# Performance work log

Hardware: AMD Instinct MI355X
Metric: run time of the kernel (lower is better)

Reference implementation:

```python
import jax, jax.numpy as jnp
import numpy as np

B, D, C, N = 8, 49, 512, 12
BN_EPS = 1e-5
SCALE = (C // 2) ** -0.5


def bn_train(x, axes):
    # training-mode batchnorm, gamma=1 beta=0 (per bn_init / default init)
    m = jnp.mean(x, axis=axes, keepdims=True)
    v = jnp.var(x, axis=axes, keepdims=True)
    return (x - m) * jax.lax.rsqrt(v + BN_EPS)


def l2norm(x):
    n = jnp.linalg.norm(x, axis=-1, keepdims=True)
    return x / jnp.maximum(n, 1e-12)


def cross_attn(y, xkv, wq, bq, wk, bk, wv, bv):
    q = y @ wq + bq
    k = xkv @ wk + bk
    v = xkv @ wv + bv
    a = jax.nn.softmax(jnp.einsum('...ik,...jk->...ij', q, k) * SCALE, axis=-1)
    return a @ v


def _gnn_layer(xv, ed, wa, wb, we, wu, wv):
    # incidence-matrix einsums reduce to repeat (end-gather) / tile (start-gather)
    res = xv
    agg = jnp.repeat(xv @ wa, N, axis=1) + jnp.tile(xv @ wb, (1, N, 1)) + ed @ we
    ed = ed + jax.nn.relu(bn_train(agg, (0, 2)))
    e = jax.nn.sigmoid(ed).reshape(-1, N, N, C)
    e = jax.nn.softmax(e, axis=2).reshape(-1, N * N, C)
    uj = jnp.tile(xv @ wv, (1, N, 1))
    msg = (e * uj).reshape(-1, N, N, C).sum(axis=2) / N  # scatter via end.T
    xv = jax.nn.relu(res + bn_train(xv @ wu + msg, (0, 2)))
    return xv, ed


def setup_inputs() -> dict:
    ks = iter(jax.random.split(jax.random.key(0), 64))

    def nrm(shape, scale=0.02):
        return jax.random.normal(next(ks), shape, dtype=jnp.float32) * scale

    g = float(np.sqrt(2.0 / C))
    inp = {'x': jax.random.normal(next(ks), (B, D, C), dtype=jnp.float32)}
    inp['Wc'] = nrm((N, C, C))
    inp['bc'] = nrm((N, C), 0.01)
    for p in ('fam', 'arm'):
        inp[p + '_wq'] = nrm((C, C // 2))
        inp[p + '_bq'] = nrm((C // 2,), 0.01)
        inp[p + '_wk'] = nrm((C, C // 2))
        inp[p + '_bk'] = nrm((C // 2,), 0.01)
        inp[p + '_wv'] = nrm((C, C))
        inp[p + '_bv'] = nrm((C,), 0.01)
    inp['ep_w'] = nrm((C, C))
    inp['ep_b'] = nrm((C,), 0.01)
    for nm in ('g_wa1', 'g_wb1', 'g_we1', 'g_wu1', 'g_wv1',
               'g_wa2', 'g_wb2', 'g_we2', 'g_wu2', 'g_wv2'):
        inp[nm] = nrm((C, C), g)
    inp['sc'] = nrm((N, C), float(np.sqrt(6.0 / (N + C))))
    inp['efc_w'] = nrm((C, 4), float(np.sqrt(6.0 / (C + 4))))
    inp['efc_b'] = nrm((4,), 0.01)
    return inp


def reference(x, Wc, bc,
              fam_wq, fam_bq, fam_wk, fam_bk, fam_wv, fam_bv,
              arm_wq, arm_bq, arm_wk, arm_bk, arm_wv, arm_bv,
              ep_w, ep_b,
              g_wa1, g_wb1, g_we1, g_wu1, g_wv1,
              g_wa2, g_wb2, g_we2, g_wu2, g_wv2,
              sc, efc_w, efc_b):
    b = x.shape[0]
    # per-class LinearBlocks (fc -> BN -> ReLU), vectorized over classes
    h = jnp.einsum('bdc,nco->bndo', x, Wc) + bc[None, :, None, :]
    f_u = jax.nn.relu(bn_train(h, (0, 2)))          # (b, N, D, C)
    f_v = f_u.mean(axis=2)                           # (b, N, C)
    # GEM edge extractor
    gf = jnp.broadcast_to(x[:, None], (b, N, D, C))
    feat = cross_attn(f_u, gf, fam_wq, fam_bq, fam_wk, fam_bk, fam_wv, fam_bv)
    feat_end = jnp.repeat(feat, N, axis=1)           # (b, N*N, D, C): edge (i,j) -> node i
    feat_start = jnp.tile(feat, (1, N, 1, 1))        # edge (i,j) -> node j
    feat = cross_attn(feat_start, feat_end, arm_wq, arm_bq, arm_wk, arm_bk, arm_wv, arm_bv)
    f_e = bn_train(feat @ ep_w + ep_b, (0, 2, 3)).mean(axis=2)  # (b, N*N, C)
    # cosine-similarity adjacency mask (detached), digraph-normalized
    si = l2norm(jax.lax.stop_gradient(f_v))
    adj = jnp.einsum('bik,bjk->bij', si, si)
    dis = jnp.sum(adj, axis=-1) ** -0.5
    mask = (adj * dis[:, :, None] * dis[:, None, :]).reshape(b, N * N, 1)
    f_e = f_e * mask
    # two GNN message-passing layers
    f_v, f_e = _gnn_layer(f_v, f_e, g_wa1, g_wb1, g_we1, g_wu1, g_wv1)
    f_v, f_e = _gnn_layer(f_v, f_e, g_wa2, g_wb2, g_we2, g_wu2, g_wv2)
    # cosine classifier + edge fc
    scn = l2norm(jax.nn.relu(sc))
    cl = jnp.sum(l2norm(f_v) * scn[None], axis=-1)   # (b, N)
    cl_edge = f_e @ efc_w + efc_b                    # (b, N*N, 4)
    return cl, cl_edge
```

## Files before the change

kernel.cpp:

```cpp
#include <hip/hip_runtime.h>
#include <math.h>

namespace {

constexpr int B = 8, D = 49, C = 512, N = 12, H = 256, E = 144;
constexpr int M_BD  = B * D;
constexpr int M_BND = B * N * D;
constexpr float BN_EPS = 1e-5f;
constexpr float ATT_SCALE = 0.0625f;

typedef __attribute__((ext_vector_type(4))) float  floatx4;
typedef __attribute__((ext_vector_type(8))) short  shortx8;

__device__ inline unsigned short f2bf(float f) {
  unsigned u = __float_as_uint(f);
  return (unsigned short)((u + 0x7fffu + ((u >> 16) & 1u)) >> 16);
}
__device__ inline float bf2f(unsigned short u) {
  return __uint_as_float(((unsigned)u) << 16);
}

__device__ inline void gload16(const unsigned short* g, unsigned short* l) {
  __builtin_amdgcn_global_load_lds(
      (const __attribute__((address_space(1))) void*)g,
      (__attribute__((address_space(3))) void*)l, 16, 0, 0);
}

struct TCJobs {
  const float* src[28];
  unsigned short* dst[28];
  int nn[28];
};

__global__ __launch_bounds__(256)
void tcast_k(TCJobs jobs)
{
  const int z = blockIdx.z;
  const float* src = jobs.src[z];
  unsigned short* dst = jobs.dst[z];
  const int Nn = jobs.nn[z];
  const int tx = blockIdx.x, ty = blockIdx.y;
  if (tx * 32 >= Nn) return;
  __shared__ float t[32][33];
  const int tid = threadIdx.x;
  const int lr = tid >> 5, lc = tid & 31;
#pragma unroll
  for (int p = 0; p < 4; ++p) {
    int k = ty * 32 + p * 8 + lr;
    t[p * 8 + lr][lc] = src[(long long)k * Nn + tx * 32 + lc];
  }
  __syncthreads();
#pragma unroll
  for (int p = 0; p < 4; ++p) {
    int n = tx * 32 + p * 8 + lr;
    dst[(long long)n * 512 + ty * 32 + lc] = f2bf(t[lc][p * 8 + lr]);
  }
}

__global__ __launch_bounds__(256)
void castrow_k(const float* __restrict__ x, unsigned short* __restrict__ xb,
               const float* __restrict__ awv, unsigned short* __restrict__ armwvb,
               const float* __restrict__ bk, const float* __restrict__ bv,
               const float* __restrict__ bq2, const float* __restrict__ bk2,
               const float* __restrict__ arm_bv, const float* __restrict__ epw,
               const float* __restrict__ epb,
               float* __restrict__ kvbias, float* __restrict__ qkvbias)
{
  int idx = blockIdx.x * 256 + threadIdx.x;
  const int n1 = M_BD * C / 8;
  const int n2 = n1 + C * C / 8;
  if (idx < n1) {
    int i8 = idx * 8;
    float4 a = *reinterpret_cast<const float4*>(x + i8);
    float4 b = *reinterpret_cast<const float4*>(x + i8 + 4);
    shortx8 o;
    o[0]=(short)f2bf(a.x); o[1]=(short)f2bf(a.y); o[2]=(short)f2bf(a.z); o[3]=(short)f2bf(a.w);
    o[4]=(short)f2bf(b.x); o[5]=(short)f2bf(b.y); o[6]=(short)f2bf(b.z); o[7]=(short)f2bf(b.w);
    *reinterpret_cast<shortx8*>(xb + i8) = o;
  } else if (idx < n2) {
    int i8 = (idx - n1) * 8;
    float4 a = *reinterpret_cast<const float4*>(awv + i8);
    float4 b = *reinterpret_cast<const float4*>(awv + i8 + 4);
    shortx8 o;
    o[0]=(short)f2bf(a.x); o[1]=(short)f2bf(a.y); o[2]=(short)f2bf(a.z); o[3]=(short)f2bf(a.w);
    o[4]=(short)f2bf(b.x); o[5]=(short)f2bf(b.y); o[6]=(short)f2bf(b.z); o[7]=(short)f2bf(b.w);
    *reinterpret_cast<shortx8*>(armwvb + i8) = o;
  } else if (idx >= 58112 && idx < 58624) {
    int c = idx - 58112;
    float s = epb[c];
    for (int k = 0; k < C; ++k) s = fmaf(arm_bv[k], epw[k * C + c], s);
    qkvbias[512 + c] = s;
  }
  if (idx < 256) { kvbias[idx] = bk[idx]; qkvbias[idx] = bq2[idx]; qkvbias[256 + idx] = bk2[idx]; }
  if (idx < 512) kvbias[256 + idx] = bv[idx];
}

__device__ __forceinline__
void gemm64_body(const void* __restrict__ Ain, const unsigned short* __restrict__ Bt,
                 const float* __restrict__ bp, float* __restrict__ co,
                 unsigned short* __restrict__ cb,
                 int M, int Nn, int K, int lda, int ldb, int ldc, int abf,
                 int bx, int by)
{
  const float* Af = abf ? nullptr : (const float*)Ain;
  const unsigned short* Ab = abf ? (const unsigned short*)Ain : nullptr;

  __shared__ short As[64 * 72];
  __shared__ short Bs[64 * 72];

  const int tid = threadIdx.x;
  const int row0 = bx * 64, col0 = by * 64;
  const int wid = tid >> 6, lane = tid & 63;
  const int wr = wid >> 1, wc = wid & 1;
  const int lr = lane & 15, lg = lane >> 4;

  floatx4 acc00 = {0.f,0.f,0.f,0.f}, acc01 = {0.f,0.f,0.f,0.f};
  floatx4 acc10 = {0.f,0.f,0.f,0.f}, acc11 = {0.f,0.f,0.f,0.f};

  const int r = tid >> 2, seg = tid & 3;
  const int gr = row0 + r, gn = col0 + r;
  short* aw = &As[r * 72 + seg * 16];
  short* bw = &Bs[r * 72 + seg * 16];
  const shortx8 zz = {0,0,0,0,0,0,0,0};

  for (int k0 = 0; k0 < K; k0 += 64) {
    shortx8 w0, w1;
    if (gr < M) {
      if (abf) {
        const shortx8* ap = reinterpret_cast<const shortx8*>(Ab + (long long)gr * lda + seg * 16 + k0);
        w0 = ap[0]; w1 = ap[1];
      } else {
        const float4* ap = reinterpret_cast<const float4*>(Af + (long long)gr * lda + seg * 16 + k0);
        float4 fa0 = ap[0], fa1 = ap[1], fa2 = ap[2], fa3 = ap[3];
        w0[0]=(short)f2bf(fa0.x); w0[1]=(short)f2bf(fa0.y); w0[2]=(short)f2bf(fa0.z); w0[3]=(short)f2bf(fa0.w);
        w0[4]=(short)f2bf(fa1.x); w0[5]=(short)f2bf(fa1.y); w0[6]=(short)f2bf(fa1.z); w0[7]=(short)f2bf(fa1.w);
        w1[0]=(short)f2bf(fa2.x); w1[1]=(short)f2bf(fa2.y); w1[2]=(short)f2bf(fa2.z); w1[3]=(short)f2bf(fa2.w);
        w1[4]=(short)f2bf(fa3.x); w1[5]=(short)f2bf(fa3.y); w1[6]=(short)f2bf(fa3.z); w1[7]=(short)f2bf(fa3.w);
      }
    } else { w0 = zz; w1 = zz; }
    const shortx8* bp8 = reinterpret_cast<const shortx8*>(Bt + (long long)gn * ldb + seg * 16 + k0);
    shortx8 b0v = bp8[0];
    shortx8 b1v = bp8[1];

    __syncthreads();
    *reinterpret_cast<shortx8*>(aw)     = w0;
    *reinterpret_cast<shortx8*>(aw + 8) = w1;
    *reinterpret_cast<shortx8*>(bw)     = b0v;
// ... 30 lines not shown
                if (okB) co[(long long)ra * ldc + colB] = v01; }
      if (cb) { if (okA) cb[(long long)ra * ldc + colA] = f2bf(v00);
                if (okB) cb[(long long)ra * ldc + colB] = f2bf(v01); }
    }
    if (rb < M) {
      if (co) { if (okA) co[(long long)rb * ldc + colA] = v10;
                if (okB) co[(long long)rb * ldc + colB] = v11; }
      if (cb) { if (okA) cb[(long long)rb * ldc + colA] = f2bf(v10);
                if (okB) cb[(long long)rb * ldc + colB] = f2bf(v11); }
    }
  }
}

__global__ __launch_bounds__(256)
void gemm_mfma(const void* __restrict__ Ain, const unsigned short* __restrict__ Bt,
               const float* __restrict__ bias, float* __restrict__ Co,
               unsigned short* __restrict__ Cb,
               int M, int Nn, int K, int lda, int ldb, int ldc, int abf,
               long long sA, long long sB, long long sBias, long long sC)
{
  const int z = blockIdx.z;
  const void* A = abf ? (const void*)((const unsigned short*)Ain + z * sA)
                      : (const void*)((const float*)Ain + z * sA);
  gemm64_body(A, Bt + z * sB, bias ? bias + z * sBias : nullptr,
              Co ? Co + z * sC : nullptr, Cb ? Cb + z * sC : nullptr,
              M, Nn, K, lda, ldb, ldc, abf, blockIdx.x, blockIdx.y);
}

struct GJob {
  const void* A; const unsigned short* B; const float* bias;
  float* Co; unsigned short* Cb;
  int M, Nn, K, lda, ldb, ldc, abf, tx;
};
struct GJobs { GJob j[3]; int ends[3]; int n; };

__global__ __launch_bounds__(256)
void gemm_jobs(GJobs js)
{
  const int bid = blockIdx.x;
#pragma unroll
  for (int q = 0; q < 3; ++q) {
    if (q < js.n && bid < js.ends[q]) {
      int start = q ? js.ends[q - 1] : 0;
      int local = bid - start;
      const GJob& J = js.j[q];
      gemm64_body(J.A, J.B, J.bias, J.Co, J.Cb,
                  J.M, J.Nn, J.K, J.lda, J.ldb, J.ldc, J.abf,
                  local % J.tx, local / J.tx);
      return;
    }
  }
}

__global__ __launch_bounds__(256)
void gemm128g(const unsigned short* __restrict__ Ab, const unsigned short* __restrict__ Bt,
              const float* __restrict__ bias, float* __restrict__ Co,
              unsigned short* __restrict__ Cb,
              int M, int Nn, int K, int lda, int ldb, int ldc,
              long long sA, long long sB, long long sBias, long long sC)
{
  const int z = blockIdx.z;
  Ab += z * sA; Bt += z * sB;
  float* co = Co ? Co + z * sC : nullptr;
  unsigned short* cb = Cb ? Cb + z * sC : nullptr;
  const float* bp = bias ? bias + z * sBias : nullptr;

  __shared__ unsigned short As[128 * 64];
  __shared__ unsigned short Bs[128 * 64];

  const int tid = threadIdx.x;
  const int row0 = blockIdx.x * 128, col0 = blockIdx.y * 128;
  const int wid = tid >> 6, lane = tid & 63;
  const int wr = wid >> 1, wc = wid & 1;
  const int lr = lane & 15, lg = lane >> 4;

  floatx4 acc[4][4];
#pragma unroll
  for (int mf = 0; mf < 4; ++mf)
#pragma unroll
    for (int nf = 0; nf < 4; ++nf) acc[mf][nf] = floatx4{0.f,0.f,0.f,0.f};

  const int rsub = tid >> 3;
  const int csub = (tid & 7) * 8;

  for (int k0 = 0; k0 < K; k0 += 64) {
    __syncthreads();
#pragma unroll
    for (int it = 0; it < 4; ++it) {
      int r = it * 32 + rsub;
      gload16(Ab + (long long)(row0 + r) * lda + k0 + csub, As + it * 2048 + tid * 8);
      gload16(Bt + (long long)(col0 + r) * ldb + k0 + csub, Bs + it * 2048 + tid * 8);
    }
    __syncthreads();

#pragma unroll
    for (int kt = 0; kt < 2; ++kt) {
      shortx8 af[4], bf[4];
#pragma unroll
      for (int mf = 0; mf < 4; ++mf)
        af[mf] = *reinterpret_cast<const shortx8*>(&As[(wr*64 + mf*16 + lr) * 64 + kt*32 + lg*8]);
#pragma unroll
      for (int nf = 0; nf < 4; ++nf)
        bf[nf] = *reinterpret_cast<const shortx8*>(&Bs[(wc*64 + nf*16 + lr) * 64 + kt*32 + lg*8]);
#pragma unroll
      for (int mf = 0; mf < 4; ++mf)
#pragma unroll
        for (int nf = 0; nf < 4; ++nf)
          acc[mf][nf] = __builtin_amdgcn_mfma_f32_16x16x32_bf16(af[mf], bf[nf], acc[mf][nf], 0, 0, 0);
    }
  }

#pragma unroll
  for (int nf = 0; nf < 4; ++nf) {
    const int col = col0 + wc * 64 + nf * 16 + lr;
    if (col >= Nn) continue;
    const float bv = bp ? bp[col] : 0.f;
#pragma unroll
    for (int mf = 0; mf < 4; ++mf) {
      const int rbase = row0 + wr * 64 + mf * 16 + lg * 4;
#pragma unroll
      for (int jj = 0; jj < 4; ++jj) {
        int row = rbase + jj;
        if (row >= M) continue;
        float v = acc[mf][nf][jj] + bv;
        if (co) co[(long long)row * ldc + col] = v;
        if (cb) cb[(long long)row * ldc + col] = f2bf(v);
      }
    }
  }
}

__global__ __launch_bounds__(256)
void bn_stats_part(const float* __restrict__ h, float* __restrict__ ps,
                   float* __restrict__ pq)
{
  int idx = blockIdx.x * 256 + threadIdx.x;
  int n = idx >> 9, c = idx & 511;
  int slice = blockIdx.y;
  const float* p = h + (long long)n * M_BD * C + (long long)slice * 49 * C + c;
  float s = 0.f, q = 0.f;
  for (int rr = 0; rr < 49; ++rr) { float v = p[(long long)rr * C]; s += v; q += v * v; }
  ps[slice * (N * C) + idx] = s;
  pq[slice * (N * C) + idx] = q;
}

__global__ __launch_bounds__(256)
void fu_fv(const float* __restrict__ h, const float* __restrict__ ps,
           const float* __restrict__ pq, unsigned short* __restrict__ fub,
           float* __restrict__ fv)
{
  const int bid = blockIdx.x;
  const int b = bid / N, n = bid % N;
  const int c = blockIdx.y * 256 + threadIdx.x;
  const int idx = n * C + c;
  float s = 0.f, q = 0.f;
#pragma unroll
  for (int sl = 0; sl < 8; ++sl) { s += ps[sl * (N * C) + idx]; q += pq[sl * (N * C) + idx]; }
  float m = s / (float)M_BD;
  float rv = rsqrtf(q / (float)M_BD - m * m + BN_EPS);
  float acc = 0.f;
  for (int d = 0; d < D; ++d) {
    float v = h[((long long)n * M_BD + b * D + d) * C + c];
    v = fmaxf((v - m) * rv, 0.f);
    fub[((long long)bid * D + d) * C + c] = f2bf(v);
    acc += v;
  }
  fv[(long long)bid * C + c] = acc * (1.0f / (float)D);
}

__global__ __launch_bounds__(256)
void softvxt_k(const float* __restrict__ Sf, unsigned short* __restrict__ Ppb,
               const unsigned short* __restrict__ kvx, unsigned short* __restrict__ vxtb)
{
  const int tid = threadIdx.x;
  if (blockIdx.x < 19) {
    int row = blockIdx.x * 256 + tid;
    if (row >= M_BND) return;
    const float* p = Sf + (long long)row * 49;
    float v[49];
    float m = -1e30f;
#pragma unroll
    for (int j = 0; j < 49; ++j) { v[j] = p[j] * ATT_SCALE; m = fmaxf(m, v[j]); }
    float s = 0.f;
#pragma unroll
    for (int j = 0; j < 49; ++j) { v[j] = __expf(v[j] - m); s += v[j]; }
    float inv = 1.f / s;
    unsigned short* o = Ppb + (long long)row * 64;
#pragma unroll
    for (int j = 0; j < 49; ++j) o[j] = f2bf(v[j] * inv);
#pragma unroll
    for (int j = 49; j < 64; ++j) o[j] = 0;
    return;
  }
  const int i = blockIdx.x - 19;
  const int b = i >> 3, cc = i & 7;
  __shared__ unsigned short t[49][65];
  for (int idx = tid; idx < 49 * 64; idx += 256) {
    int rr = idx >> 6, k = idx & 63;
    t[rr][k] = kvx[(long long)(b * 49 + rr) * 768 + 256 + cc * 64 + k];
  }
  __syncthreads();
  for (int idx = tid; idx < 64 * 64; idx += 256) {
    int n = idx >> 6, kk = idx & 63;
    vxtb[((long long)b * 512 + cc * 64 + n) * 64 + kk] = (kk < 49) ? t[kk][n] : (unsigned short)0;
  }
}

__global__ __launch_bounds__(256)
void edge_finish(const float* __restrict__ Sc, const float* __restrict__ G,
                 const unsigned short* __restrict__ qkvfe,
                 float* __restrict__ S1, float* __restrict__ eS)
{
  const int bid = blockIdx.x;
  const int b = bid / E, e = bid % E;
  const int i = e / N, j = e % N;
  const float* Scb = Sc + (long long)b * 588 * 588 + (long long)(j * 49) * 588 + i * 49;
  const float* Gp  = G + (long long)(b * N + i) * 2401;
  const unsigned short* Vp = qkvfe + (long long)(b * N + i) * D * 1024 + 512;

  __shared__ float aT[49][53];
  __shared__ float g[49][53];
  __shared__ unsigned short abT[64][72];
  __shared__ float ws[52];
  __shared__ float r0[4], r1[4];
  const int tid = threadIdx.x;
  const int wid = tid >> 6, lane = tid & 63;
  const int lr = lane & 15, lg = lane >> 4;

  for (int idx = tid; idx < 49 * 49; idx += 256) {
    int di = idx / 49, dj = idx - di * 49;
    aT[dj][di] = Scb[di * 588 + dj] * ATT_SCALE;
    g[di][dj] = Gp[idx];
  }
  __syncthreads();
  if (tid < D) {
    float m = -1e30f;
    for (int jj = 0; jj < D; ++jj) m = fmaxf(m, aT[jj][tid]);
    float s = 0.f;
    for (int jj = 0; jj < D; ++jj) { float ev = __expf(aT[jj][tid] - m); aT[jj][tid] = ev; s += ev; }
    float inv = 1.f / s;
    for (int jj = 0; jj < D; ++jj) aT[jj][tid] *= inv;
  }
  __syncthreads();
  for (int idx = tid; idx < 64 * 64; idx += 256) {
    int dj = idx >> 6, di = idx & 63;
    float v = (dj < D && di < D) ? aT[dj][di] : 0.f;
    abT[dj][di] = f2bf(v);
  }
  if (tid < D) {
    float s = 0.f;
    for (int di = 0; di < D; ++di) s += aT[tid][di];
    ws[tid] = s;
  }
  __syncthreads();

  floatx4 acc[4];
#pragma unroll
  for (int tk = 0; tk < 4; ++tk) acc[tk] = floatx4{0.f,0.f,0.f,0.f};
  shortx8 af0 = *reinterpret_cast<const shortx8*>(&abT[wid * 16 + lr][lg * 8]);
  shortx8 af1 = *reinterpret_cast<const shortx8*>(&abT[wid * 16 + lr][32 + lg * 8]);
#pragma unroll
  for (int tk = 0; tk < 4; ++tk) {
    shortx8 bf0v = *reinterpret_cast<const shortx8*>(&abT[tk * 16 + lr][lg * 8]);
    shortx8 bf1v = *reinterpret_cast<const shortx8*>(&abT[tk * 16 + lr][32 + lg * 8]);
    acc[tk] = __builtin_amdgcn_mfma_f32_16x16x32_bf16(af0, bf0v, acc[tk], 0, 0, 0);
    acc[tk] = __builtin_amdgcn_mfma_f32_16x16x32_bf16(af1, bf1v, acc[tk], 0, 0, 0);
  }
  float st2 = 0.f;
#pragma unroll
  for (int tk = 0; tk < 4; ++tk) {
    int kcol = tk * 16 + lr;
#pragma unroll
    for (int rg = 0; rg < 4; ++rg) {
      int jrow = wid * 16 + lg * 4 + rg;
      if (jrow < D && kcol < D) st2 = fmaf(acc[tk][rg], g[jrow][kcol], st2);
    }
  }

  float st = 0.f;
#pragma unroll
  for (int cc = 0; cc < C; cc += 256) {
    int cg = cc + tid;
    float s1 = 0.f;
    for (int dk = 0; dk < D; ++dk) s1 = fmaf(ws[dk], bf2f(Vp[dk * 1024 + cg]), s1);
    S1[(long long)bid * C + cg] = s1;
    st += s1;
  }
  for (int off = 32; off; off >>= 1) { st += __shfl_down(st, off); st2 += __shfl_down(st2, off); }
  if (lane == 0) { r0[wid] = st; r1[wid] = st2; }
  __syncthreads();
  if (tid == 0) {
    eS[bid * 2 + 0] = r0[0] + r0[1] + r0[2] + r0[3];
    eS[bid * 2 + 1] = r1[0] + r1[1] + r1[2] + r1[3];
  }
}

__global__ __launch_bounds__(256)
void mask_me_k(const float* __restrict__ fv, const float* __restrict__ eS,
               float* __restrict__ mask, float* __restrict__ me, float* __restrict__ rve)
{
  if (blockIdx.x == B) {
    int e = threadIdx.x;
    if (e < E) {
      float s = 0.f, q = 0.f;
      for (int b = 0; b < B; ++b) { s += eS[(b * E + e) * 2]; q += eS[(b * E + e) * 2 + 1]; }
      const float inv = 1.f / (float)(B * D * C);
      float m = s * inv;
      me[e] = m;
      rve[e] = rsqrtf(q * inv - m * m + BN_EPS);
    }
    return;
  }
  const int b = blockIdx.x;
  __shared__ float fl[N][C];
  __shared__ float adj[N][N];
  __shared__ float nrm[N];
  __shared__ float dis[N];
  const int tid = threadIdx.x;
  for (int idx = tid; idx < N * C; idx += 256)
    fl[idx / C][idx % C] = fv[(long long)b * N * C + idx];
  __syncthreads();
  if (tid < N * N) {
    int i = tid / N, j = tid % N;
    float s = 0.f;
    for (int k = 0; k < C; ++k) s += fl[i][k] * fl[j][k];
    adj[i][j] = s;
  }
  __syncthreads();
  if (tid < N) nrm[tid] = fmaxf(sqrtf(adj[tid][tid]), 1e-12f);
  __syncthreads();
  if (tid < N * N) {
    int i = tid / N, j = tid % N;
    adj[i][j] = adj[i][j] / (nrm[i] * nrm[j]);
  }
  __syncthreads();
  if (tid < N) {
    float s = 0.f;
    for (int j = 0; j < N; ++j) s += adj[tid][j];
    dis[tid] = rsqrtf(s);
  }
  __syncthreads();
  if (tid < N * N) {
    int i = tid / N, j = tid % N;
    mask[b * E + tid] = adj[i][j] * dis[i] * dis[j];
  }
}

__global__ void fe_k(const float* __restrict__ S1, const float* __restrict__ me,
                     const float* __restrict__ rve, const float* __restrict__ mask,
                     float* __restrict__ fe)
{
  long long idx = (long long)blockIdx.x * 256 + threadIdx.x;
  if (idx >= (long long)B * E * C) return;
  long long be = idx / C;
  int e = (int)(be % E);
  fe[idx] = (S1[idx] * (1.0f / (float)D) - me[e]) * rve[e] * mask[be];
}

__global__ __launch_bounds__(256)
void agg_stats(const float* __restrict__ ABUV, const float* __restrict__ EW,
               float* __restrict__ mu_e, float* __restrict__ rs_e)
{
  const int e = blockIdx.x;
  const int i = e / N, j = e % N;
  const int tid = threadIdx.x;
  float s = 0.f, q = 0.f;
  for (int idx = tid; idx < B * C; idx += 256) {
    int b = idx >> 9, c = idx & 511;
    float v = ABUV[(long long)(b * N + i) * 2048 + c]
            + ABUV[(long long)(b * N + j) * 2048 + 512 + c]
            + EW[((long long)b * E + e) * C + c];
    s += v; q += v * v;
  }
  for (int off = 32; off; off >>= 1) { s += __shfl_down(s, off); q += __shfl_down(q, off); }
  __shared__ float r0[4], r1[4];
  int wid = tid >> 6, lane = tid & 63;
  if (lane == 0) { r0[wid] = s; r1[wid] = q; }
  __syncthreads();
  if (tid == 0) {
    float ss = r0[0] + r0[1] + r0[2] + r0[3];
    float qq = r1[0] + r1[1] + r1[2] + r1[3];
    float m = ss / (float)(B * C);
    mu_e[e] = m;
    rs_e[e] = rsqrtf(qq / (float)(B * C) - m * m + BN_EPS);
  }
}

__global__ __launch_bounds__(256)
void edmsg_k(float* __restrict__ fe, const float* __restrict__ ABUV,
             const float* __restrict__ EW, const float* __restrict__ mu_e,
             const float* __restrict__ rs_e, float* __restrict__ pre)
{
  const int bid = blockIdx.x;
  const int b = bid / N, i = bid % N;
  const int tid = threadIdx.x;
  for (int c = tid; c < C; c += 256) {
    float ai = ABUV[(long long)(b * N + i) * 2048 + c];
    float sv[N];
    float m = -1e30f;
#pragma unroll
    for (int jn = 0; jn < N; ++jn) {
      int e = i * N + jn;
      float v = ai + ABUV[(long long)(b * N + jn) * 2048 + 512 + c]
              + EW[((long long)b * E + e) * C + c];
      v = (v - mu_e[e]) * rs_e[e];
      float ed = fe[((long long)b * E + e) * C + c] + fmaxf(v, 0.f);
      fe[((long long)b * E + e) * C + c] = ed;
      float sg = 1.f / (1.f + __expf(-ed));
      sv[jn] = sg; m = fmaxf(m, sg);
    }
    float sum = 0.f;
#pragma unroll
    for (int jn = 0; jn < N; ++jn) { float ev = __expf(sv[jn] - m); sv[jn] = ev; sum += ev; }
    float acc = 0.f;
#pragma unroll
    for (int jn = 0; jn < N; ++jn)
      acc = fmaf(sv[jn], ABUV[(long long)(b * N + jn) * 2048 + 1536 + c], acc);
    acc /= (sum * (float)N);
    pre[(long long)bid * C + c] = ABUV[(long long)bid * 2048 + 1024 + c] + acc;
  }
}

__global__ __launch_bounds__(256)
void node_part(const float* __restrict__ pre, float* __restrict__ nps,
               float* __restrict__ npq)
{
  const int i = blockIdx.x, b = blockIdx.y;
  const int tid = threadIdx.x;
  float v0 = pre[(long long)(b * N + i) * C + tid];
  float v1 = pre[(long long)(b * N + i) * C + 256 + tid];
  float s = v0 + v1, q = v0 * v0 + v1 * v1;
  for (int off = 32; off; off >>= 1) { s += __shfl_down(s, off); q += __shfl_down(q, off); }
  __shared__ float r0[4], r1[4];
  int wid = tid >> 6, lane = tid & 63;
  if (lane == 0) { r0[wid] = s; r1[wid] = q; }
  __syncthreads();
  if (tid == 0) {
    nps[i * B + b] = r0[0] + r0[1] + r0[2] + r0[3];
    npq[i * B + b] = r1[0] + r1[1] + r1[2] + r1[3];
  }
}

__global__ void xv_update(float* __restrict__ xv, const float* __restrict__ pre,
                          const float* __restrict__ nps, const float* __restrict__ npq)
{
  long long idx = (long long)blockIdx.x * 256 + threadIdx.x;
  if (idx >= (long long)B * N * C) return;
  int i = (int)((idx / C) % N);
  float s = 0.f, q = 0.f;
#pragma unroll
  for (int bb = 0; bb < B; ++bb) { s += nps[i * B + bb]; q += npq[i * B + bb]; }
  float mu = s * (1.f / (float)(B * C));
  float rs = rsqrtf(q * (1.f / (float)(B * C)) - mu * mu + BN_EPS);
  float v = xv[idx] + (pre[idx] - mu) * rs;
  xv[idx] = fmaxf(v, 0.f);
}

__global__ __launch_bounds__(256)
void out_k(const float* __restrict__ xv, const float* __restrict__ sc,
           const float* __restrict__ ed, const float* __restrict__ w,
           const float* __restrict__ bias, float* __restrict__ out)
{
  const int bid = blockIdx.x;
  const int tid = threadIdx.x;
  int wid = tid >> 6, lane = tid & 63;
  if (bid < B * N) {
    const int b = bid / N, i = bid % N;
    float sxx = 0.f, sss = 0.f, sxs = 0.f;
    for (int c = tid; c < C; c += 256) {
      float xvv = xv[(long long)(b * N + i) * C + c];
      float scv = fmaxf(sc[i * C + c], 0.f);
      sxx += xvv * xvv; sss += scv * scv; sxs += xvv * scv;
    }
    for (int off = 32; off; off >>= 1) {
      sxx += __shfl_down(sxx, off);
      sss += __shfl_down(sss, off);
      sxs += __shfl_down(sxs, off);
    }
    __shared__ float r0[4], r1[4], r2[4];
    if (lane == 0) { r0[wid] = sxx; r1[wid] = sss; r2[wid] = sxs; }
    __syncthreads();
    if (tid == 0) {
      float a = r0[0] + r0[1] + r0[2] + r0[3];
      float s = r1[0] + r1[1] + r1[2] + r1[3];
      float p = r2[0] + r2[1] + r2[2] + r2[3];
      float nx = fmaxf(sqrtf(a), 1e-12f);
      float ns = fmaxf(sqrtf(s), 1e-12f);
      out[b * N + i] = p / (nx * ns);
// ... 17 lines not shown
    __shared__ float r[4][4];
    if (lane == 0) { r[wid][0] = a0; r[wid][1] = a1; r[wid][2] = a2; r[wid][3] = a3; }
    __syncthreads();
    if (tid < 4) {
      float s = r[0][tid] + r[1][tid] + r[2][tid] + r[3][tid];
      out[B * N + eb * 4 + tid] = s + bias[tid];
    }
  }
}

}

extern "C" void kernel_launch(void* const* d_in, const int* in_sizes, int n_in,
                              void* d_out, int out_size, void* d_ws, size_t ws_size,
                              hipStream_t stream)
{
  (void)in_sizes; (void)n_in; (void)out_size; (void)ws_size;
  const float* x      = (const float*)d_in[0];
  const float* Wc     = (const float*)d_in[1];
  const float* bc     = (const float*)d_in[2];
  const float* fam_wq = (const float*)d_in[3];
  const float* fam_bq = (const float*)d_in[4];
  const float* fam_wk = (const float*)d_in[5];
  const float* fam_bk = (const float*)d_in[6];
  const float* fam_wv = (const float*)d_in[7];
  const float* fam_bv = (const float*)d_in[8];
  const float* arm_wq = (const float*)d_in[9];
  const float* arm_bq = (const float*)d_in[10];
  const float* arm_wk = (const float*)d_in[11];
  const float* arm_bk = (const float*)d_in[12];
  const float* arm_wv = (const float*)d_in[13];
  const float* arm_bv = (const float*)d_in[14];
  const float* ep_w   = (const float*)d_in[15];
  const float* ep_b   = (const float*)d_in[16];
  const float* gw[10] = {
    (const float*)d_in[17], (const float*)d_in[18], (const float*)d_in[19],
    (const float*)d_in[20], (const float*)d_in[21],
    (const float*)d_in[22], (const float*)d_in[23], (const float*)d_in[24],
    (const float*)d_in[25], (const float*)d_in[26]};
  const float* sc     = (const float*)d_in[27];
  const float* efc_w  = (const float*)d_in[28];
  const float* efc_b  = (const float*)d_in[29];
  float* out = (float*)d_out;

  char* wsb = (char*)d_ws;
  size_t off = 0;
  auto allocf = [&](size_t n) { float* p = (float*)(wsb + off); off += ((n * 4 + 255) / 256) * 256; return p; };
  auto allocu = [&](size_t n) { unsigned short* p = (unsigned short*)(wsb + off); off += ((n * 2 + 255) / 256) * 256; return p; };

  float* region_a = allocf(2766336);
  float* h_t = region_a;
  float* Sc  = region_a;

  float* bnp_s = allocf(49152);
  float* bnp_q = allocf(49152);
  float* f_v   = allocf(49152);
  float* Sf    = allocf(230496);
  float* Gm    = allocf(230496);
  float* S1    = allocf(589824);
  float* fe    = allocf(589824);
  float* EW    = allocf(589824);
  float* eS    = allocf(2304);
  float* me    = allocf(144);
  float* rve   = allocf(144);
  float* mask  = allocf(1152);
  float* ABUV  = allocf(196608);
  float* pre   = allocf(49152);
  float* mu_e  = allocf(144);
  float* rs_e  = allocf(144);
  float* nps   = allocf(96);
  float* npq   = allocf(96);
  float* kvbias  = allocf(768);
  float* qkvbias = allocf(1024);

  unsigned short* Wct    = allocu(3145728);
  unsigned short* famqt  = allocu(131072);
  unsigned short* kvwt   = allocu(393216);
  unsigned short* qkw2t  = allocu(524288);
  unsigned short* epwt   = allocu(262144);
  unsigned short* armwvb = allocu(262144);
  unsigned short* wet0   = allocu(262144);
  unsigned short* wet1   = allocu(262144);
  unsigned short* ABUVt0 = allocu(1048576);
  unsigned short* ABUVt1 = allocu(1048576);
  unsigned short* xb     = allocu(262144);
  unsigned short* fub    = allocu(2408448);
  unsigned short* q1b    = allocu(1204224);
  unsigned short* kxvx_b = allocu(350208);
  unsigned short* Ppb    = allocu(301056);
  unsigned short* vxtb   = allocu(262144);
  unsigned short* featb  = allocu(2424832);
  unsigned short* qkvfe  = allocu(4915200);

  dim3 blk(256);

  TCJobs tj{};
  int jn = 0;
  for (int n = 0; n < 12; ++n) { tj.src[jn] = Wc + (size_t)n * C * C; tj.dst[jn] = Wct + (size_t)n * C * C; tj.nn[jn] = C; ++jn; }
  tj.src[jn] = fam_wq; tj.dst[jn] = famqt;             tj.nn[jn] = H; ++jn;
  tj.src[jn] = fam_wk; tj.dst[jn] = kvwt;              tj.nn[jn] = H; ++jn;
  tj.src[jn] = fam_wv; tj.dst[jn] = kvwt + 256 * 512;  tj.nn[jn] = C; ++jn;
  tj.src[jn] = arm_wq; tj.dst[jn] = qkw2t;             tj.nn[jn] = H; ++jn;
  tj.src[jn] = arm_wk; tj.dst[jn] = qkw2t + 256 * 512; tj.nn[jn] = H; ++jn;
  tj.src[jn] = ep_w;   tj.dst[jn] = epwt;              tj.nn[jn] = C; ++jn;
  tj.src[jn] = gw[2];  tj.dst[jn] = wet0;              tj.nn[jn] = C; ++jn;
  tj.src[jn] = gw[7];  tj.dst[jn] = wet1;              tj.nn[jn] = C; ++jn;
  tj.src[jn] = gw[0];  tj.dst[jn] = ABUVt0;               tj.nn[jn] = C; ++jn;
  tj.src[jn] = gw[1];  tj.dst[jn] = ABUVt0 + 1 * C * C;   tj.nn[jn] = C; ++jn;
  tj.src[jn] = gw[3];  tj.dst[jn] = ABUVt0 + 2 * C * C;   tj.nn[jn] = C; ++jn;
  tj.src[jn] = gw[4];  tj.dst[jn] = ABUVt0 + 3 * C * C;   tj.nn[jn] = C; ++jn;
  tj.src[jn] = gw[5];  tj.dst[jn] = ABUVt1;               tj.nn[jn] = C; ++jn;
  tj.src[jn] = gw[6];  tj.dst[jn] = ABUVt1 + 1 * C * C;   tj.nn[jn] = C; ++jn;
  tj.src[jn] = gw[8];  tj.dst[jn] = ABUVt1 + 2 * C * C;   tj.nn[jn] = C; ++jn;
  tj.src[jn] = gw[9];  tj.dst[jn] = ABUVt1 + 3 * C * C;   tj.nn[jn] = C; ++jn;
  tcast_k<<<dim3(16, 16, 28), blk, 0, stream>>>(tj);

  castrow_k<<<dim3(229), blk, 0, stream>>>(x, xb, arm_wv, armwvb,
      fam_bk, fam_bv, arm_bq, arm_bk, arm_bv, ep_w, ep_b, kvbias, qkvbias);

  gemm128g<<<dim3(4, 4, 12), blk, 0, stream>>>(xb, Wct, bc, h_t, nullptr,
      M_BD, C, C, C, C, C, 0LL, (long long)C * C, (long long)C, (long long)M_BD * C);
  bn_stats_part<<<dim3(24, 8), blk, 0, stream>>>(h_t, bnp_s, bnp_q);
  fu_fv<<<dim3(B * N, 2), blk, 0, stream>>>(h_t, bnp_s, bnp_q, fub, f_v);

  {
    GJobs js{};
    js.j[0] = {fub,  famqt,  fam_bq, nullptr, q1b,            M_BND, H,   C, C, C, H,   1, 74};
    js.j[1] = {xb,   kvwt,   kvbias, nullptr, kxvx_b,         M_BD,  768, C, C, C, 768, 1, 7};
    js.j[2] = {epwt, armwvb, nullptr, nullptr, qkw2t + 512 * 512, C,  C,   C, C, C, C,   1, 8};
    js.ends[0] = 296; js.ends[1] = 380; js.ends[2] = 444; js.n = 3;
    gemm_jobs<<<dim3(444), blk, 0, stream>>>(js);
  }
  gemm_mfma<<<dim3(10, 1, 8), blk, 0, stream>>>(q1b, kxvx_b, nullptr, Sf, nullptr,
      588, 49, H, H, 768, 49, 1, 588LL * 256, 49LL * 768, 0LL, 588LL * 49);
  softvxt_k<<<dim3(19 + 64), blk, 0, stream>>>(Sf, Ppb, kxvx_b, vxtb);
  gemm_mfma<<<dim3(10, 8, 8), blk, 0, stream>>>(Ppb, vxtb, nullptr, nullptr, featb,
      588, C, 64, 64, 64, C, 1, 588LL * 64, 512LL * 64, 0LL, 588LL * 512);

  gemm128g<<<dim3(37, 8, 1), blk, 0, stream>>>(featb, qkw2t, qkvbias, nullptr, qkvfe,
      M_BND, 1024, C, C, C, 1024, 0, 0, 0, 0);

  gemm128g<<<dim3(5, 5, 8), blk, 0, stream>>>(qkvfe, qkvfe + 256, nullptr, Sc, nullptr,
      588, 588, H, 1024, 1024, 588, 588LL * 1024, 588LL * 1024, 0LL, 588LL * 588);
  gemm_mfma<<<dim3(1, 1, 96), blk, 0, stream>>>(qkvfe + 512, qkvfe + 512, nullptr, Gm, nullptr,
      D, D, C, 1024, 1024, D, 1, 49LL * 1024, 49LL * 1024, 0LL, 49LL * 49);

  edge_finish<<<dim3(B * E), blk, 0, stream>>>(Sc, Gm, qkvfe, S1, eS);
  mask_me_k<<<dim3(B + 1), blk, 0, stream>>>(f_v, eS, mask, me, rve);
  fe_k<<<dim3((B * E * C + 255) / 256), blk, 0, stream>>>(S1, me, rve, mask, fe);

  for (int L = 0; L < 2; ++L) {
    const unsigned short* ABUVt = L ? ABUVt1 : ABUVt0;
    const unsigned short* wet   = L ? wet1 : wet0;
    {
      GJobs js{};
      js.j[0] = {f_v, ABUVt, nullptr, ABUV, nullptr, B * N, 2048, C, C, C, 2048, 0, 2};
      js.j[1] = {fe,  wet,   nullptr, EW,   nullptr, B * E, C,    C, C, C, C,    0, 18};
      js.ends[0] = 64; js.ends[1] = 208; js.ends[2] = 208; js.n = 2;
      gemm_jobs<<<dim3(208), blk, 0, stream>>>(js);
    }
    agg_stats<<<dim3(E), blk, 0, stream>>>(ABUV, EW, mu_e, rs_e);
    edmsg_k<<<dim3(B * N), blk, 0, stream>>>(fe, ABUV, EW, mu_e, rs_e, pre);
    node_part<<<dim3(N, B), blk, 0, stream>>>(pre, nps, npq);
    xv_update<<<dim3((B * N * C + 255) / 256), blk, 0, stream>>>(f_v, pre, nps, npq);
  }

  out_k<<<dim3(B * N + B * E), blk, 0, stream>>>(f_v, sc, fe, efc_w, efc_b, out);
}
```

Baseline: 249.9 us.

## Fuse small kernels and launches to cut launch overhead across the pipeline

Merges several small kernels into neighbouring launches. The row-cast work joins the transpose-cast grid, and the BN stats move into the first GEMM epilogue via shared-memory atomics. The mask computation joins the softmax kernel, the Sc and Gm GEMMs share one launch, and the me/rve computation folds into fe_k. node_part stats fold into edmsg_k, and edge_finish vectorises its bf16 V loads. This removes around six launches and one pass over h. The costs are extra epilogue work in the GEMM and some redundant per-block stat recomputation in fe_k.

```diff
diff --git a/kernel.cpp b/kernel.cpp
--- a/kernel.cpp
+++ b/kernel.cpp
@@ -33,16 +33,53 @@
 };
 
 __global__ __launch_bounds__(256)
-void tcast_k(TCJobs jobs)
+void tcast_k(TCJobs jobs,
+             const float* __restrict__ x, unsigned short* __restrict__ xb,
+             const float* __restrict__ awv, unsigned short* __restrict__ armwvb,
+             const float* __restrict__ bk, const float* __restrict__ bv,
+             const float* __restrict__ bq2, const float* __restrict__ bk2,
+             const float* __restrict__ arm_bv, const float* __restrict__ epw,
+             const float* __restrict__ epb,
+             float* __restrict__ kvbias, float* __restrict__ qkvbias)
 {
   const int z = blockIdx.z;
+  const int tid = threadIdx.x;
+  if (z == 28) {
+    int idx = (blockIdx.y * 16 + blockIdx.x) * 256 + tid;
+    const int n1 = M_BD * C / 8;
+    const int n2 = n1 + C * C / 8;
+    if (idx < n1) {
+      int i8 = idx * 8;
+      float4 a = *reinterpret_cast<const float4*>(x + i8);
+      float4 b = *reinterpret_cast<const float4*>(x + i8 + 4);
+      shortx8 o;
+      o[0]=(short)f2bf(a.x); o[1]=(short)f2bf(a.y); o[2]=(short)f2bf(a.z); o[3]=(short)f2bf(a.w);
+      o[4]=(short)f2bf(b.x); o[5]=(short)f2bf(b.y); o[6]=(short)f2bf(b.z); o[7]=(short)f2bf(b.w);
+      *reinterpret_cast<shortx8*>(xb + i8) = o;
+    } else if (idx < n2) {
+      int i8 = (idx - n1) * 8;
+      float4 a = *reinterpret_cast<const float4*>(awv + i8);
+      float4 b = *reinterpret_cast<const float4*>(awv + i8 + 4);
+      shortx8 o;
+      o[0]=(short)f2bf(a.x); o[1]=(short)f2bf(a.y); o[2]=(short)f2bf(a.z); o[3]=(short)f2bf(a.w);
+      o[4]=(short)f2bf(b.x); o[5]=(short)f2bf(b.y); o[6]=(short)f2bf(b.z); o[7]=(short)f2bf(b.w);
+      *reinterpret_cast<shortx8*>(armwvb + i8) = o;
+    } else if (idx >= 58112 && idx < 58624) {
+      int c = idx - 58112;
+      float s = epb[c];
+      for (int k = 0; k < C; ++k) s = fmaf(arm_bv[k], epw[k * C + c], s);
+      qkvbias[512 + c] = s;
+    }
+    if (idx < 256) { kvbias[idx] = bk[idx]; qkvbias[idx] = bq2[idx]; qkvbias[256 + idx] = bk2[idx]; }
+    if (idx < 512) kvbias[256 + idx] = bv[idx];
+    return;
+  }
   const float* src = jobs.src[z];
   unsigned short* dst = jobs.dst[z];
   const int Nn = jobs.nn[z];
   const int tx = blockIdx.x, ty = blockIdx.y;
   if (tx * 32 >= Nn) return;
   __shared__ float t[32][33];
-  const int tid = threadIdx.x;
   const int lr = tid >> 5, lc = tid & 31;
 #pragma unroll
   for (int p = 0; p < 4; ++p) {
@@ -55,44 +92,6 @@
     int n = tx * 32 + p * 8 + lr;
     dst[(long long)n * 512 + ty * 32 + lc] = f2bf(t[lc][p * 8 + lr]);
   }
-}
-
-__global__ __launch_bounds__(256)
-void castrow_k(const float* __restrict__ x, unsigned short* __restrict__ xb,
-               const float* __restrict__ awv, unsigned short* __restrict__ armwvb,
-               const float* __restrict__ bk, const float* __restrict__ bv,
-               const float* __restrict__ bq2, const float* __restrict__ bk2,
-               const float* __restrict__ arm_bv, const float* __restrict__ epw,
-               const float* __restrict__ epb,
-               float* __restrict__ kvbias, float* __restrict__ qkvbias)
-{
-  int idx = blockIdx.x * 256 + threadIdx.x;
-  const int n1 = M_BD * C / 8;
-  const int n2 = n1 + C * C / 8;
-  if (idx < n1) {
-    int i8 = idx * 8;
-    float4 a = *reinterpret_cast<const float4*>(x + i8);
-    float4 b = *reinterpret_cast<const float4*>(x + i8 + 4);
-    shortx8 o;
-    o[0]=(short)f2bf(a.x); o[1]=(short)f2bf(a.y); o[2]=(short)f2bf(a.z); o[3]=(short)f2bf(a.w);
-    o[4]=(short)f2bf(b.x); o[5]=(short)f2bf(b.y); o[6]=(short)f2bf(b.z); o[7]=(short)f2bf(b.w);
-    *reinterpret_cast<shortx8*>(xb + i8) = o;
-  } else if (idx < n2) {
-    int i8 = (idx - n1) * 8;
-    float4 a = *reinterpret_cast<const float4*>(awv + i8);
-    float4 b = *reinterpret_cast<const float4*>(awv + i8 + 4);
-    shortx8 o;
-    o[0]=(short)f2bf(a.x); o[1]=(short)f2bf(a.y); o[2]=(short)f2bf(a.z); o[3]=(short)f2bf(a.w);
-    o[4]=(short)f2bf(b.x); o[5]=(short)f2bf(b.y); o[6]=(short)f2bf(b.z); o[7]=(short)f2bf(b.w);
-    *reinterpret_cast<shortx8*>(armwvb + i8) = o;
-  } else if (idx >= 58112 && idx < 58624) {
-    int c = idx - 58112;
-    float s = epb[c];
-    for (int k = 0; k < C; ++k) s = fmaf(arm_bv[k], epw[k * C + c], s);
-    qkvbias[512 + c] = s;
-  }
-  if (idx < 256) { kvbias[idx] = bk[idx]; qkvbias[idx] = bq2[idx]; qkvbias[256 + idx] = bk2[idx]; }
-  if (idx < 512) kvbias[256 + idx] = bv[idx];
 }
 
 __device__ __forceinline__
@@ -229,24 +228,17 @@
   }
 }
 
-__global__ __launch_bounds__(256)
-void gemm128g(const unsigned short* __restrict__ Ab, const unsigned short* __restrict__ Bt,
-              const float* __restrict__ bias, float* __restrict__ Co,
-              unsigned short* __restrict__ Cb,
-              int M, int Nn, int K, int lda, int ldb, int ldc,
-              long long sA, long long sB, long long sBias, long long sC)
-{
-  const int z = blockIdx.z;
-  Ab += z * sA; Bt += z * sB;
-  float* co = Co ? Co + z * sC : nullptr;
-  unsigned short* cb = Cb ? Cb + z * sC : nullptr;
-  const float* bp = bias ? bias + z * sBias : nullptr;
-
+__device__ __forceinline__
+void g128_body(const unsigned short* __restrict__ Ab, const unsigned short* __restrict__ Bt,
+               const float* __restrict__ bp, float* __restrict__ co,
+               unsigned short* __restrict__ cb, float* __restrict__ psb, float* __restrict__ pqb,
+               int M, int Nn, int K, int lda, int ldb, int ldc, int bx, int by)
+{
   __shared__ unsigned short As[128 * 64];
   __shared__ unsigned short Bs[128 * 64];
 
   const int tid = threadIdx.x;
-  const int row0 = blockIdx.x * 128, col0 = blockIdx.y * 128;
+  const int row0 = bx * 128, col0 = by * 128;
   const int wid = tid >> 6, lane = tid & 63;
   const int wr = wid >> 1, wc = wid & 1;
   const int lr = lane & 15, lg = lane >> 4;
@@ -305,20 +297,70 @@
       }
     }
   }
-}
-
-__global__ __launch_bounds__(256)
-void bn_stats_part(const float* __restrict__ h, float* __restrict__ ps,
-                   float* __restrict__ pq)
-{
-  int idx = blockIdx.x * 256 + threadIdx.x;
-  int n = idx >> 9, c = idx & 511;
-  int slice = blockIdx.y;
-  const float* p = h + (long long)n * M_BD * C + (long long)slice * 49 * C + c;
-  float s = 0.f, q = 0.f;
-  for (int rr = 0; rr < 49; ++rr) { float v = p[(long long)rr * C]; s += v; q += v * v; }
-  ps[slice * (N * C) + idx] = s;
-  pq[slice * (N * C) + idx] = q;
+
+  if (psb) {
+    __syncthreads();
+    float* sb = (float*)As;
+    sb[tid] = 0.f;
+    __syncthreads();
+#pragma unroll
+    for (int nf = 0; nf < 4; ++nf) {
+      const int lcol = wc * 64 + nf * 16 + lr;
+      const int col = col0 + lcol;
+      float s = 0.f, q = 0.f;
+      if (col < Nn) {
+        const float bv = bp ? bp[col] : 0.f;
+#pragma unroll
+        for (int mf = 0; mf < 4; ++mf) {
+          const int rbase = row0 + wr * 64 + mf * 16 + lg * 4;
+#pragma unroll
+          for (int jj = 0; jj < 4; ++jj) {
+            if (rbase + jj < M) { float v = acc[mf][nf][jj] + bv; s += v; q += v * v; }
+          }
+        }
+      }
+      atomicAdd(&sb[lcol], s);
+      atomicAdd(&sb[128 + lcol], q);
+    }
+    __syncthreads();
+    if (tid < 128) {
+      psb[col0 + tid] = sb[tid];
+      pqb[col0 + tid] = sb[128 + tid];
+    }
+  }
+}
+
+__global__ __launch_bounds__(256)
+void gemm128g(const unsigned short* __restrict__ Ab, const unsigned short* __restrict__ Bt,
+              const float* __restrict__ bias, float* __restrict__ Co,
+              unsigned short* __restrict__ Cb, float* __restrict__ ps, float* __restrict__ pq,
+              int M, int Nn, int K, int lda, int ldb, int ldc,
+              long long sA, long long sB, long long sBias, long long sC)
+{
+  const int z = blockIdx.z;
+  long long so = ((long long)blockIdx.x * gridDim.z + z) * ldc;
+  g128_body(Ab + z * sA, Bt + z * sB, bias ? bias + z * sBias : nullptr,
+            Co ? Co + z * sC : nullptr, Cb ? Cb + z * sC : nullptr,
+            ps ? ps + so : nullptr, pq ? pq + so : nullptr,
+            M, Nn, K, lda, ldb, ldc, blockIdx.x, blockIdx.y);
+}
+
+__global__ __launch_bounds__(256)
+void scgm_k(const unsigned short* __restrict__ qkvfe, float* __restrict__ Sc,
+            float* __restrict__ Gm)
+{
+  const int bid = blockIdx.x;
+  if (bid < 200) {
+    int z = bid / 25, rem = bid % 25;
+    g128_body(qkvfe + (long long)z * 588 * 1024, qkvfe + 256 + (long long)z * 588 * 1024,
+              nullptr, Sc + (long long)z * 588 * 588, nullptr, nullptr, nullptr,
+              588, 588, H, 1024, 1024, 588, rem % 5, rem / 5);
+  } else {
+    int z = bid - 200;
+    const unsigned short* vp = qkvfe + 512 + (long long)z * 49 * 1024;
+    gemm64_body(vp, vp, nullptr, Gm + (long long)z * 2401, nullptr,
+                D, D, C, 1024, 1024, D, 1, 0, 0);
+  }
 }
 
 __global__ __launch_bounds__(256)
@@ -332,7 +374,7 @@
   const int idx = n * C + c;
   float s = 0.f, q = 0.f;
 #pragma unroll
-  for (int sl = 0; sl < 8; ++sl) { s += ps[sl * (N * C) + idx]; q += pq[sl * (N * C) + idx]; }
+  for (int sl = 0; sl < 4; ++sl) { s += ps[sl * (N * C) + idx]; q += pq[sl * (N * C) + idx]; }
   float m = s / (float)M_BD;
   float rv = rsqrtf(q / (float)M_BD - m * m + BN_EPS);
   float acc = 0.f;
@@ -347,7 +389,8 @@
 
 __global__ __launch_bounds__(256)
 void softvxt_k(const float* __restrict__ Sf, unsigned short* __restrict__ Ppb,
-               const unsigned short* __restrict__ kvx, unsigned short* __restrict__ vxtb)
+               const unsigned short* __restrict__ kvx, unsigned short* __restrict__ vxtb,
+               const float* __restrict__ fv, float* __restrict__ maskp)
 {
   const int tid = threadIdx.x;
   if (blockIdx.x < 19) {
@@ -369,17 +412,52 @@
     for (int j = 49; j < 64; ++j) o[j] = 0;
     return;
   }
-  const int i = blockIdx.x - 19;
-  const int b = i >> 3, cc = i & 7;
-  __shared__ unsigned short t[49][65];
-  for (int idx = tid; idx < 49 * 64; idx += 256) {
-    int rr = idx >> 6, k = idx & 63;
-    t[rr][k] = kvx[(long long)(b * 49 + rr) * 768 + 256 + cc * 64 + k];
-  }
-  __syncthreads();
-  for (int idx = tid; idx < 64 * 64; idx += 256) {
-    int n = idx >> 6, kk = idx & 63;
-    vxtb[((long long)b * 512 + cc * 64 + n) * 64 + kk] = (kk < 49) ? t[kk][n] : (unsigned short)0;
+  if (blockIdx.x < 83) {
+    const int i = blockIdx.x - 19;
+    const int b = i >> 3, cc = i & 7;
+    __shared__ unsigned short t[49][65];
+    for (int idx = tid; idx < 49 * 64; idx += 256) {
+      int rr = idx >> 6, k = idx & 63;
+      t[rr][k] = kvx[(long long)(b * 49 + rr) * 768 + 256 + cc * 64 + k];
+    }
+    __syncthreads();
+    for (int idx = tid; idx < 64 * 64; idx += 256) {
+      int n = idx >> 6, kk = idx & 63;
+      vxtb[((long long)b * 512 + cc * 64 + n) * 64 + kk] = (kk < 49) ? t[kk][n] : (unsigned short)0;
+    }
+    return;
+  }
+  const int b = blockIdx.x - 83;
+  __shared__ float fl[N][C];
+  __shared__ float adj[N][N];
+  __shared__ float nrm[N];
+  __shared__ float dis[N];
+  for (int idx = tid; idx < N * C; idx += 256)
+    fl[idx / C][idx % C] = fv[(long long)b * N * C + idx];
+  __syncthreads();
+  if (tid < N * N) {
+    int i = tid / N, j = tid % N;
+    float s = 0.f;
+    for (int k = 0; k < C; ++k) s += fl[i][k] * fl[j][k];
+    adj[i][j] = s;
+  }
+  __syncthreads();
+  if (tid < N) nrm[tid] = fmaxf(sqrtf(adj[tid][tid]), 1e-12f);
+  __syncthreads();
+  if (tid < N * N) {
+    int i = tid / N, j = tid % N;
+    adj[i][j] = adj[i][j] / (nrm[i] * nrm[j]);
+  }
+  __syncthreads();
+  if (tid < N) {
+    float s = 0.f;
+    for (int j = 0; j < N; ++j) s += adj[tid][j];
+    dis[tid] = rsqrtf(s);
+  }
+  __syncthreads();
+  if (tid < N * N) {
+    int i = tid / N, j = tid % N;
+    maskp[b * E + tid] = adj[i][j] * dis[i] * dis[j];
   }
 }
 
@@ -454,15 +532,18 @@
     }
   }
 
-  float st = 0.f;
-#pragma unroll
-  for (int cc = 0; cc < C; cc += 256) {
-    int cg = cc + tid;
-    float s1 = 0.f;
-    for (int dk = 0; dk < D; ++dk) s1 = fmaf(ws[dk], bf2f(Vp[dk * 1024 + cg]), s1);
-    S1[(long long)bid * C + cg] = s1;
-    st += s1;
-  }
+  const unsigned* Vp32 = reinterpret_cast<const unsigned*>(Vp);
+  float s1a = 0.f, s1b = 0.f;
+  for (int dk = 0; dk < D; ++dk) {
+    unsigned u = Vp32[dk * 512 + tid];
+    float w = ws[dk];
+    s1a = fmaf(w, bf2f((unsigned short)(u & 0xffffu)), s1a);
+    s1b = fmaf(w, bf2f((unsigned short)(u >> 16)), s1b);
+  }
+  S1[(long long)bid * C + 2 * tid]     = s1a;
+  S1[(long long)bid * C + 2 * tid + 1] = s1b;
+  float st = s1a + s1b;
+
   for (int off = 32; off; off >>= 1) { st += __shfl_down(st, off); st2 += __shfl_down(st2, off); }
   if (lane == 0) { r0[wid] = st; r1[wid] = st2; }
   __syncthreads();
@@ -473,65 +554,25 @@
 }
 
 __global__ __launch_bounds__(256)
-void mask_me_k(const float* __restrict__ fv, const float* __restrict__ eS,
-               float* __restrict__ mask, float* __restrict__ me, float* __restrict__ rve)
-{
-  if (blockIdx.x == B) {
-    int e = threadIdx.x;
-    if (e < E) {
-      float s = 0.f, q = 0.f;
-      for (int b = 0; b < B; ++b) { s += eS[(b * E + e) * 2]; q += eS[(b * E + e) * 2 + 1]; }
-      const float inv = 1.f / (float)(B * D * C);
-      float m = s * inv;
-      me[e] = m;
-      rve[e] = rsqrtf(q * inv - m * m + BN_EPS);
-    }
-    return;
-  }
-  const int b = blockIdx.x;
-  __shared__ float fl[N][C];
-  __shared__ float adj[N][N];
-  __shared__ float nrm[N];
-  __shared__ float dis[N];
-  const int tid = threadIdx.x;
-  for (int idx = tid; idx < N * C; idx += 256)
-    fl[idx / C][idx % C] = fv[(long long)b * N * C + idx];
-  __syncthreads();
-  if (tid < N * N) {
-    int i = tid / N, j = tid % N;
-    float s = 0.f;
-    for (int k = 0; k < C; ++k) s += fl[i][k] * fl[j][k];
-    adj[i][j] = s;
-  }
-  __syncthreads();
-  if (tid < N) nrm[tid] = fmaxf(sqrtf(adj[tid][tid]), 1e-12f);
-  __syncthreads();
-  if (tid < N * N) {
-    int i = tid / N, j = tid % N;
-    adj[i][j] = adj[i][j] / (nrm[i] * nrm[j]);
-  }
-  __syncthreads();
-  if (tid < N) {
-    float s = 0.f;
-    for (int j = 0; j < N; ++j) s += adj[tid][j];
-    dis[tid] = rsqrtf(s);
-  }
-  __syncthreads();
-  if (tid < N * N) {
-    int i = tid / N, j = tid % N;
-    mask[b * E + tid] = adj[i][j] * dis[i] * dis[j];
-  }
-}
-
-__global__ void fe_k(const float* __restrict__ S1, const float* __restrict__ me,
-                     const float* __restrict__ rve, const float* __restrict__ mask,
-                     float* __restrict__ fe)
-{
-  long long idx = (long long)blockIdx.x * 256 + threadIdx.x;
-  if (idx >= (long long)B * E * C) return;
-  long long be = idx / C;
+void fe_k(const float* __restrict__ S1, const float* __restrict__ eS,
+          const float* __restrict__ maskp, float* __restrict__ fe)
+{
+  __shared__ float csh[3];
+  long long idx0 = (long long)blockIdx.x * 256;
+  long long be = idx0 / C;
   int e = (int)(be % E);
-  fe[idx] = (S1[idx] * (1.0f / (float)D) - me[e]) * rve[e] * mask[be];
+  if (threadIdx.x == 0) {
+    float s = 0.f, q = 0.f;
+    for (int b = 0; b < B; ++b) { s += eS[(b * E + e) * 2]; q += eS[(b * E + e) * 2 + 1]; }
+    const float inv = 1.f / (float)(B * D * C);
+    float m = s * inv;
+    csh[0] = m;
+    csh[1] = rsqrtf(q * inv - m * m + BN_EPS);
+    csh[2] = maskp[be];
+  }
+  __syncthreads();
+  long long idx = idx0 + threadIdx.x;
+  fe[idx] = (S1[idx] * (1.0f / (float)D) - csh[0]) * csh[1] * csh[2];
 }
 
 __global__ __launch_bounds__(256)
@@ -566,11 +607,13 @@
 __global__ __launch_bounds__(256)
 void edmsg_k(float* __restrict__ fe, const float* __restrict__ ABUV,
              const float* __restrict__ EW, const float* __restrict__ mu_e,
-             const float* __restrict__ rs_e, float* __restrict__ pre)
+             const float* __restrict__ rs_e, float* __restrict__ pre,
+             float* __restrict__ nps, float* __restrict__ npq)
 {
   const int bid = blockIdx.x;
   const int b = bid / N, i = bid % N;
   const int tid = threadIdx.x;
+  float ls = 0.f, lq = 0.f;
   for (int c = tid; c < C; c += 256) {
     float ai = ABUV[(long long)(b * N + i) * 2048 + c];
     float sv[N];
@@ -594,23 +637,14 @@
     for (int jn = 0; jn < N; ++jn)
       acc = fmaf(sv[jn], ABUV[(long long)(b * N + jn) * 2048 + 1536 + c], acc);
     acc /= (sum * (float)N);
-    pre[(long long)bid * C + c] = ABUV[(long long)bid * 2048 + 1024 + c] + acc;
-  }
-}
-
-__global__ __launch_bounds__(256)
-void node_part(const float* __restrict__ pre, float* __restrict__ nps,
-               float* __restrict__ npq)
-{
-  const int i = blockIdx.x, b = blockIdx.y;
-  const int tid = threadIdx.x;
-  float v0 = pre[(long long)(b * N + i) * C + tid];
-  float v1 = pre[(long long)(b * N + i) * C + 256 + tid];
-  float s = v0 + v1, q = v0 * v0 + v1 * v1;
-  for (int off = 32; off; off >>= 1) { s += __shfl_down(s, off); q += __shfl_down(q, off); }
+    float pv = ABUV[(long long)bid * 2048 + 1024 + c] + acc;
+    pre[(long long)bid * C + c] = pv;
+    ls += pv; lq += pv * pv;
+  }
+  for (int off = 32; off; off >>= 1) { ls += __shfl_down(ls, off); lq += __shfl_down(lq, off); }
   __shared__ float r0[4], r1[4];
   int wid = tid >> 6, lane = tid & 63;
-  if (lane == 0) { r0[wid] = s; r1[wid] = q; }
+  if (lane == 0) { r0[wid] = ls; r1[wid] = lq; }
   __syncthreads();
   if (tid == 0) {
     nps[i * B + b] = r0[0] + r0[1] + r0[2] + r0[3];
@@ -734,8 +768,8 @@
   float* h_t = region_a;
   float* Sc  = region_a;
 
-  float* bnp_s = allocf(49152);
-  float* bnp_q = allocf(49152);
+  float* bnp_s = allocf(24576);
+  float* bnp_q = allocf(24576);
   float* f_v   = allocf(49152);
   float* Sf    = allocf(230496);
   float* Gm    = allocf(230496);
@@ -743,8 +777,6 @@
   float* fe    = allocf(589824);
   float* EW    = allocf(589824);
   float* eS    = allocf(2304);
-  float* me    = allocf(144);
-  float* rve   = allocf(144);
   float* mask  = allocf(1152);
   float* ABUV  = allocf(196608);
   float* pre   = allocf(49152);
@@ -795,14 +827,11 @@
   tj.src[jn] = gw[6];  tj.dst[jn] = ABUVt1 + 1 * C * C;   tj.nn[jn] = C; ++jn;
   tj.src[jn] = gw[8];  tj.dst[jn] = ABUVt1 + 2 * C * C;   tj.nn[jn] = C; ++jn;
   tj.src[jn] = gw[9];  tj.dst[jn] = ABUVt1 + 3 * C * C;   tj.nn[jn] = C; ++jn;
-  tcast_k<<<dim3(16, 16, 28), blk, 0, stream>>>(tj);
-
-  castrow_k<<<dim3(229), blk, 0, stream>>>(x, xb, arm_wv, armwvb,
+  tcast_k<<<dim3(16, 16, 29), blk, 0, stream>>>(tj, x, xb, arm_wv, armwvb,
       fam_bk, fam_bv, arm_bq, arm_bk, arm_bv, ep_w, ep_b, kvbias, qkvbias);
 
-  gemm128g<<<dim3(4, 4, 12), blk, 0, stream>>>(xb, Wct, bc, h_t, nullptr,
+  gemm128g<<<dim3(4, 4, 12), blk, 0, stream>>>(xb, Wct, bc, h_t, nullptr, bnp_s, bnp_q,
       M_BD, C, C, C, C, C, 0LL, (long long)C * C, (long long)C, (long long)M_BD * C);
-  bn_stats_part<<<dim3(24, 8), blk, 0, stream>>>(h_t, bnp_s, bnp_q);
   fu_fv<<<dim3(B * N, 2), blk, 0, stream>>>(h_t, bnp_s, bnp_q, fub, f_v);
 
   {
@@ -815,21 +844,17 @@
   }
   gemm_mfma<<<dim3(10, 1, 8), blk, 0, stream>>>(q1b, kxvx_b, nullptr, Sf, nullptr,
       588, 49, H, H, 768, 49, 1, 588LL * 256, 49LL * 768, 0LL, 588LL * 49);
-  softvxt_k<<<dim3(19 + 64), blk, 0, stream>>>(Sf, Ppb, kxvx_b, vxtb);
+  softvxt_k<<<dim3(91), blk, 0, stream>>>(Sf, Ppb, kxvx_b, vxtb, f_v, mask);
   gemm_mfma<<<dim3(10, 8, 8), blk, 0, stream>>>(Ppb, vxtb, nullptr, nullptr, featb,
       588, C, 64, 64, 64, C, 1, 588LL * 64, 512LL * 64, 0LL, 588LL * 512);
 
   gemm128g<<<dim3(37, 8, 1), blk, 0, stream>>>(featb, qkw2t, qkvbias, nullptr, qkvfe,
-      M_BND, 1024, C, C, C, 1024, 0, 0, 0, 0);
-
-  gemm128g<<<dim3(5, 5, 8), blk, 0, stream>>>(qkvfe, qkvfe + 256, nullptr, Sc, nullptr,
-      588, 588, H, 1024, 1024, 588, 588LL * 1024, 588LL * 1024, 0LL, 588LL * 588);
-  gemm_mfma<<<dim3(1, 1, 96), blk, 0, stream>>>(qkvfe + 512, qkvfe + 512, nullptr, Gm, nullptr,
-      D, D, C, 1024, 1024, D, 1, 49LL * 1024, 49LL * 1024, 0LL, 49LL * 49);
+      nullptr, nullptr, M_BND, 1024, C, C, C, 1024, 0, 0, 0, 0);
+
+  scgm_k<<<dim3(296), blk, 0, stream>>>(qkvfe, Sc, Gm);
 
   edge_finish<<<dim3(B * E), blk, 0, stream>>>(Sc, Gm, qkvfe, S1, eS);
-  mask_me_k<<<dim3(B + 1), blk, 0, stream>>>(f_v, eS, mask, me, rve);
-  fe_k<<<dim3((B * E * C + 255) / 256), blk, 0, stream>>>(S1, me, rve, mask, fe);
+  fe_k<<<dim3(2304), blk, 0, stream>>>(S1, eS, mask, fe);
 
   for (int L = 0; L < 2; ++L) {
     const unsigned short* ABUVt = L ? ABUVt1 : ABUVt0;
@@ -842,8 +867,7 @@
       gemm_jobs<<<dim3(208), blk, 0, stream>>>(js);
     }
     agg_stats<<<dim3(E), blk, 0, stream>>>(ABUV, EW, mu_e, rs_e);
-    edmsg_k<<<dim3(B * N), blk, 0, stream>>>(fe, ABUV, EW, mu_e, rs_e, pre);
-    node_part<<<dim3(N, B), blk, 0, stream>>>(pre, nps, npq);
+    edmsg_k<<<dim3(B * N), blk, 0, stream>>>(fe, ABUV, EW, mu_e, rs_e, pre, nps, npq);
     xv_update<<<dim3((B * N * C + 255) / 256), blk, 0, stream>>>(f_v, pre, nps, npq);
   }
 
```

After: 213.1 us. -14.7%, faster.
